# Kernel optimization log

Measured on AMD Instinct MI355X. Metric: run time of the kernel, lower is better.

The kernel has to match this reference:

```python
import jax, jax.numpy as jnp
import numpy as np

BN_EPS = 1e-5


def _fps(xyz, n_centers):
    """Furthest point sampling. xyz: (B,N,3) -> idx (B,n_centers) int32.
    Deterministic start at index 0 (torch version uses randint start)."""
    B, N, _ = xyz.shape
    batch_ar = jnp.arange(B)

    def step(carry, _):
        distances, farthest = carry  # (B,N), (B,)
        center = xyz[batch_ar, farthest]  # (B,3)
        d = jnp.sum((xyz - center[:, None, :]) ** 2, axis=-1)  # (B,N)
        distances = jnp.minimum(distances, d)
        new_far = jnp.argmax(distances, axis=-1)
        return (distances, new_far), farthest

    init = (jnp.full((B, N), jnp.inf, dtype=xyz.dtype),
            jnp.zeros((B,), dtype=jnp.int32))
    _, idxs = jax.lax.scan(step, init, None, length=n_centers)  # (n_centers, B)
    return idxs.T  # (B, n_centers)


def _knn_group(xyz, centers, k):
    """xyz:(B,N,3), centers:(B,M,3) -> patches (B,M,k,3) center-relative."""
    # (B,M,N) squared distances
    dists = jnp.sum((centers[:, :, None, :] - xyz[:, None, :, :]) ** 2, axis=-1)
    _, idx = jax.lax.top_k(-dists, k)  # (B,M,k) smallest distances
    # gather neighbor coords: (B,M,k,3)
    patches = jnp.take_along_axis(xyz[:, None, :, :], idx[..., None], axis=2)
    return patches - centers[:, :, None, :]


def _bn_eval(x, gamma, beta):
    # BatchNorm1d in eval mode: running_mean=0, running_var=1
    return x * (gamma / jnp.sqrt(1.0 + BN_EPS)) + beta


def _mini_pointnet(patches, W1, b1, g1, bt1, W2, b2, g2, bt2, W3, b3, g3, bt3):
    B, M, k, C = patches.shape
    x = patches.reshape(B * M * k, C)
    x = jax.nn.relu(_bn_eval(x @ W1 + b1, g1, bt1))
    x = jax.nn.relu(_bn_eval(x @ W2 + b2, g2, bt2))
    x = jax.nn.relu(_bn_eval(x @ W3 + b3, g3, bt3))
    x = x.reshape(B * M, k, -1).max(axis=1)
    return x.reshape(B, M, -1)


def setup_inputs() -> dict:
    key = jax.random.key(0)
    ks = jax.random.split(key, 8)
    B, N = 16, 16384
    embed = 256

    def lin(kk, fan_in, fan_out):
        bound = 1.0 / np.sqrt(fan_in)
        k1, k2 = jax.random.split(kk)
        W = jax.random.uniform(k1, (fan_in, fan_out), jnp.float32, -bound, bound)
        b = jax.random.uniform(k2, (fan_out,), jnp.float32, -bound, bound)
        return W, b

    W1, b1 = lin(ks[1], 3, 64)
    W2, b2 = lin(ks[2], 64, 128)
    W3, b3 = lin(ks[3], 128, embed)
    return {
        "xyz": jax.random.normal(ks[0], (B, N, 3), jnp.float32),
        "W1": W1, "b1": b1, "g1": jnp.ones((64,)), "bt1": jnp.zeros((64,)),
        "W2": W2, "b2": b2, "g2": jnp.ones((128,)), "bt2": jnp.zeros((128,)),
        "W3": W3, "b3": b3, "g3": jnp.ones((embed,)), "bt3": jnp.zeros((embed,)),
        "n_centers": 256,
        "k": 32,
    }


def reference(xyz, W1, b1, g1, bt1, W2, b2, g2, bt2, W3, b3, g3, bt3,
              n_centers, k):
    center_idx = _fps(xyz, n_centers)  # (B, M)
    centers = jnp.take_along_axis(xyz, center_idx[..., None], axis=1)  # (B,M,3)
    patches = _knn_group(xyz, centers, k)  # (B,M,k,3)
    tokens = _mini_pointnet(patches, W1, b1, g1, bt1, W2, b2, g2, bt2,
                            W3, b3, g3, bt3)
    return tokens, centers
```

## Files before the change

kernel.cpp:

```cpp
#include <hip/hip_runtime.h>

constexpr int B   = 16;
constexpr int N   = 16384;
constexpr int M   = 256;
constexpr int K   = 32;
constexpr int EMB = 256;

__device__ __forceinline__ float sqdist(float px, float py, float pz,
                                        float cx, float cy, float cz) {
  float dx = __fsub_rn(px, cx);
  float dy = __fsub_rn(py, cy);
  float dz = __fsub_rn(pz, cz);
  return __fadd_rn(__fadd_rn(__fmul_rn(dx, dx), __fmul_rn(dy, dy)),
                   __fmul_rn(dz, dz));
}

constexpr int FPS_T = 1024;
constexpr int PPT = N / FPS_T;

__global__ __launch_bounds__(FPS_T) void fps_kernel(
    const float* __restrict__ xyz, float* __restrict__ centers) {
  const int b = blockIdx.x;
  const int tid = threadIdx.x;
  const float* base = xyz + (size_t)b * N * 3;

  float px[PPT], py[PPT], pz[PPT], dist[PPT];
#pragma unroll
  for (int j = 0; j < PPT; ++j) {
    int n = tid + j * FPS_T;
    px[j] = base[n * 3 + 0];
    py[j] = base[n * 3 + 1];
    pz[j] = base[n * 3 + 2];
    dist[j] = __builtin_inff();
  }

  __shared__ float s_c[3];
  __shared__ float s_wv[FPS_T / 64];
  __shared__ int s_wi[FPS_T / 64];
  if (tid == 0) { s_c[0] = base[0]; s_c[1] = base[1]; s_c[2] = base[2]; }
  __syncthreads();

  for (int it = 0; it < M; ++it) {
    const float cx = s_c[0], cy = s_c[1], cz = s_c[2];
    if (tid == 0) {
      float* co = centers + ((size_t)b * M + it) * 3;
      co[0] = cx; co[1] = cy; co[2] = cz;
    }
    float bv = -1.0f;
    int bi = 0x7FFFFFFF;
#pragma unroll
    for (int j = 0; j < PPT; ++j) {
      float d = sqdist(px[j], py[j], pz[j], cx, cy, cz);
      float nd = fminf(dist[j], d);
      dist[j] = nd;
      if (nd > bv) { bv = nd; bi = tid + j * FPS_T; }
    }
#pragma unroll
    for (int mm = 32; mm >= 1; mm >>= 1) {
      float ov = __shfl_xor(bv, mm, 64);
      int oi = __shfl_xor(bi, mm, 64);
      if (ov > bv || (ov == bv && oi < bi)) { bv = ov; bi = oi; }
    }
    if ((tid & 63) == 0) { s_wv[tid >> 6] = bv; s_wi[tid >> 6] = bi; }
    __syncthreads();
    if (tid < 64) {
      float v = (tid < FPS_T / 64) ? s_wv[tid] : -1.0f;
      int i = (tid < FPS_T / 64) ? s_wi[tid] : 0x7FFFFFFF;
#pragma unroll
      for (int mm = 32; mm >= 1; mm >>= 1) {
        float ov = __shfl_xor(v, mm, 64);
        int oi = __shfl_xor(i, mm, 64);
        if (ov > v || (ov == v && oi < i)) { v = ov; i = oi; }
      }
      if (tid == 0) {
        s_c[0] = base[(size_t)i * 3 + 0];
        s_c[1] = base[(size_t)i * 3 + 1];
        s_c[2] = base[(size_t)i * 3 + 2];
      }
    }
    __syncthreads();
  }
}

constexpr int KT = 256;
constexpr int CAP = 512;
constexpr int NBUCKET = 1024;

__global__ __launch_bounds__(KT) void knn_kernel(
    const float* __restrict__ xyz, const float* __restrict__ centers,
    float* __restrict__ patches) {
  const int blk = blockIdx.x;
  const int b = blk >> 8;
  const int tid = threadIdx.x;
  const float* base = xyz + (size_t)b * N * 3;

  __shared__ int hist[NBUCKET];
  __shared__ unsigned cb[CAP];
  __shared__ int ci[CAP];
  __shared__ int s_nin, s_ncand, s_tb;
  __shared__ int s_wsum[KT / 64];
  __shared__ float s_cc[3];

  if (tid == 0) {
    const float* c = centers + (size_t)blk * 3;
    s_cc[0] = c[0]; s_cc[1] = c[1]; s_cc[2] = c[2];
    s_nin = 0; s_ncand = 0;
  }
  for (int i = tid; i < NBUCKET; i += KT) hist[i] = 0;
  __syncthreads();

  const float cx = s_cc[0], cy = s_cc[1], cz = s_cc[2];

  for (int n = tid; n < N; n += KT) {
    float d = sqdist(base[n * 3], base[n * 3 + 1], base[n * 3 + 2], cx, cy, cz);
    atomicAdd(&hist[__float_as_uint(d) >> 21], 1);
  }
  __syncthreads();

  int h0[4];
  int loc = 0;
#pragma unroll
  for (int i = 0; i < 4; ++i) { h0[i] = hist[tid * 4 + i]; loc += h0[i]; }
  int lane = tid & 63, wid = tid >> 6;
  int scan = loc;
  for (int off = 1; off < 64; off <<= 1) {
    int o = __shfl_up(scan, off, 64);
    if (lane >= off) scan += o;
  }
  if (lane == 63) s_wsum[wid] = scan;
  __syncthreads();
  int woff = 0;
  for (int w = 0; w < wid; ++w) woff += s_wsum[w];
  int c0 = woff + scan - loc;
#pragma unroll
  for (int i = 0; i < 4; ++i) {
    int c1 = c0 + h0[i];
    if (c0 < K && c1 >= K) s_tb = tid * 4 + i;
    c0 = c1;
  }
  __syncthreads();
  const int tb = s_tb;
  const unsigned lo = (unsigned)tb << 21;
  const unsigned hi = (unsigned)(tb + 1) << 21;

  for (int n = tid; n < N; n += KT) {
    float x = base[n * 3], y = base[n * 3 + 1], z = base[n * 3 + 2];
    float d = sqdist(x, y, z, cx, cy, cz);
    unsigned bits = __float_as_uint(d);
    if (bits < lo) {
      int pos = atomicAdd(&s_nin, 1);
      float* p = patches + ((size_t)blk * K + pos) * 3;
      p[0] = __fsub_rn(x, cx); p[1] = __fsub_rn(y, cy); p[2] = __fsub_rn(z, cz);
    } else if (bits < hi) {
      int q = atomicAdd(&s_ncand, 1);
      if (q < CAP) { cb[q] = bits; ci[q] = n; }
    }
  }
  __syncthreads();

  const int nin = s_nin;
  const int ncand = min(s_ncand, CAP);
  const int nsel = K - nin;
  for (int j = tid; j < ncand; j += KT) {
    unsigned bj = cb[j];
    int ij = ci[j];
    int rank = 0;
    for (int i2 = 0; i2 < ncand; ++i2) {
      unsigned bv = cb[i2];
      int iv = ci[i2];
      rank += (bv < bj || (bv == bj && iv < ij)) ? 1 : 0;
    }
    if (rank < nsel) {
      float x = base[ij * 3], y = base[ij * 3 + 1], z = base[ij * 3 + 2];
      float* p = patches + ((size_t)blk * K + nin + rank) * 3;
      p[0] = __fsub_rn(x, cx); p[1] = __fsub_rn(y, cy); p[2] = __fsub_rn(z, cz);
    }
  }
}

constexpr int MT = 128;

__global__ __launch_bounds__(MT) void mlp_kernel(
    const float* __restrict__ patches,
    const float* __restrict__ W1, const float* __restrict__ b1,
    const float* __restrict__ g1, const float* __restrict__ bt1,
    const float* __restrict__ W2, const float* __restrict__ b2,
    const float* __restrict__ g2, const float* __restrict__ bt2,
    const float* __restrict__ W3, const float* __restrict__ b3,
    const float* __restrict__ g3, const float* __restrict__ bt3,
    float* __restrict__ tokens) {
  const int pm = blockIdx.x;
  const int tid = threadIdx.x;
  __shared__ float xs[3][K];
  __shared__ float h1s[64 * K];
  __shared__ float h2s[128 * K];
  __shared__ float pms[2][EMB];

  const float* patch = patches + (size_t)pm * (K * 3);
  if (tid < 96) xs[tid % 3][tid / 3] = patch[tid];
  __syncthreads();

  const int cg = tid & 63;
  const int half = tid >> 6;
  const int pt0 = half * 16;
  const float rs = 1.0f / sqrtf(1.0f + 1e-5f);

  {
    const int c = cg;
    const float w0 = W1[c], w1 = W1[64 + c], w2 = W1[128 + c];
    const float bb = b1[c];
    const float sc = g1[c] * rs, be = bt1[c];
    float o[16];
#pragma unroll
    for (int p = 0; p < 16; ++p) {
      int pt = pt0 + p;
      float a = xs[0][pt] * w0 + xs[1][pt] * w1 + xs[2][pt] * w2 + bb;
      o[p] = fmaxf(a * sc + be, 0.0f);
    }
    const int so = (c & 7) << 2;
#pragma unroll
    for (int p4 = 0; p4 < 16; p4 += 4) {
      *(float4*)&h1s[c * K + ((pt0 + p4) ^ so)] =
          make_float4(o[p4], o[p4 + 1], o[p4 + 2], o[p4 + 3]);
    }
  }
  __syncthreads();

  {
    const int c = cg * 2;
    float acc0[16], acc1[16];
    const float bb0 = b2[c], bb1 = b2[c + 1];
#pragma unroll
    for (int p = 0; p < 16; ++p) { acc0[p] = bb0; acc1[p] = bb1; }
    for (int k = 0; k < 64; ++k) {
      const float2 w = *(const float2*)(W2 + k * 128 + c);
      const int so = (k & 7) << 2;
      float4 x0 = *(const float4*)&h1s[k * K + ((pt0 + 0) ^ so)];
      float4 x1 = *(const float4*)&h1s[k * K + ((pt0 + 4) ^ so)];
      float4 x2 = *(const float4*)&h1s[k * K + ((pt0 + 8) ^ so)];
      float4 x3 = *(const float4*)&h1s[k * K + ((pt0 + 12) ^ so)];
      float xv[16] = {x0.x, x0.y, x0.z, x0.w, x1.x, x1.y, x1.z, x1.w,
                      x2.x, x2.y, x2.z, x2.w, x3.x, x3.y, x3.z, x3.w};
#pragma unroll
      for (int p = 0; p < 16; ++p) {
        acc0[p] += xv[p] * w.x;
        acc1[p] += xv[p] * w.y;
      }
    }
    const float sc0 = g2[c] * rs, be0 = bt2[c];
    const float sc1 = g2[c + 1] * rs, be1 = bt2[c + 1];
    float o0[16], o1[16];
#pragma unroll
    for (int p = 0; p < 16; ++p) {
      o0[p] = fmaxf(acc0[p] * sc0 + be0, 0.0f);
      o1[p] = fmaxf(acc1[p] * sc1 + be1, 0.0f);
    }
    const int soa = (c & 7) << 2, sob = ((c + 1) & 7) << 2;
#pragma unroll
    for (int p4 = 0; p4 < 16; p4 += 4) {
      *(float4*)&h2s[c * K + ((pt0 + p4) ^ soa)] =
          make_float4(o0[p4], o0[p4 + 1], o0[p4 + 2], o0[p4 + 3]);
      *(float4*)&h2s[(c + 1) * K + ((pt0 + p4) ^ sob)] =
          make_float4(o1[p4], o1[p4 + 1], o1[p4 + 2], o1[p4 + 3]);
    }
  }
  __syncthreads();

  {
    const int c = cg * 4;
    float acc[4][16];
#pragma unroll
    for (int i = 0; i < 4; ++i) {
      const float bb = b3[c + i];
#pragma unroll
      for (int p = 0; p < 16; ++p) acc[i][p] = bb;
    }
    for (int k = 0; k < 128; ++k) {
      const float4 w = *(const float4*)(W3 + (size_t)k * 256 + c);
      const int so = (k & 7) << 2;
      float4 x0 = *(const float4*)&h2s[k * K + ((pt0 + 0) ^ so)];
      float4 x1 = *(const float4*)&h2s[k * K + ((pt0 + 4) ^ so)];
      float4 x2 = *(const float4*)&h2s[k * K + ((pt0 + 8) ^ so)];
      float4 x3 = *(const float4*)&h2s[k * K + ((pt0 + 12) ^ so)];
      float xv[16] = {x0.x, x0.y, x0.z, x0.w, x1.x, x1.y, x1.z, x1.w,
                      x2.x, x2.y, x2.z, x2.w, x3.x, x3.y, x3.z, x3.w};
#pragma unroll
      for (int p = 0; p < 16; ++p) {
        acc[0][p] += xv[p] * w.x;
        acc[1][p] += xv[p] * w.y;
        acc[2][p] += xv[p] * w.z;
        acc[3][p] += xv[p] * w.w;
      }
    }
#pragma unroll
    for (int i = 0; i < 4; ++i) {
      const float sc = g3[c + i] * rs, be = bt3[c + i];
      float mx = 0.0f;
#pragma unroll
      for (int p = 0; p < 16; ++p)
        mx = fmaxf(mx, fmaxf(acc[i][p] * sc + be, 0.0f));
      pms[half][c + i] = mx;
    }
  }
  __syncthreads();

  {
    const int c2 = tid * 2;
    float* to = tokens + (size_t)pm * EMB;
    to[c2] = fmaxf(pms[0][c2], pms[1][c2]);
    to[c2 + 1] = fmaxf(pms[0][c2 + 1], pms[1][c2 + 1]);
  }
}

extern "C" void kernel_launch(void* const* d_in, const int* in_sizes, int n_in,
                              void* d_out, int out_size, void* d_ws,
                              size_t ws_size, hipStream_t stream) {
  const float* xyz = (const float*)d_in[0];
  const float* W1 = (const float*)d_in[1];
  const float* b1 = (const float*)d_in[2];
  const float* g1 = (const float*)d_in[3];
  const float* bt1 = (const float*)d_in[4];
  const float* W2 = (const float*)d_in[5];
  const float* b2 = (const float*)d_in[6];
  const float* g2 = (const float*)d_in[7];
  const float* bt2 = (const float*)d_in[8];
  const float* W3 = (const float*)d_in[9];
  const float* b3 = (const float*)d_in[10];
  const float* g3 = (const float*)d_in[11];
  const float* bt3 = (const float*)d_in[12];

  float* tokens = (float*)d_out;
  float* centers = tokens + (size_t)B * M * EMB;
  float* patches = (float*)d_ws;

  fps_kernel<<<B, FPS_T, 0, stream>>>(xyz, centers);
  knn_kernel<<<B * M, KT, 0, stream>>>(xyz, centers, patches);
  mlp_kernel<<<B * M, MT, 0, stream>>>(patches, W1, b1, g1, bt1, W2, b2, g2,
                                       bt2, W3, b3, g3, bt3, tokens);
}
```

Before: 863.0 us.

## Cut FPS to one barrier per iteration with double-buffered shared reduction

The furthest-point-sampling kernel now uses 512 threads with 32 points each and double-buffers the per-wave argmax results in shared memory. Every thread redundantly reduces the wave results and loads the new center from global memory, so the second barrier and the shared-memory center broadcast go away. The inner argmax keeps a local slot index chosen by select and computes the global index afterwards. In exchange, more points per thread raise register pressure and every thread does a redundant 8-way reduction and a global load each iteration.

```diff
diff --git a/kernel.cpp b/kernel.cpp
--- a/kernel.cpp
+++ b/kernel.cpp
@@ -15,70 +15,74 @@
                    __fmul_rn(dz, dz));
 }
 
-constexpr int FPS_T = 1024;
-constexpr int PPT = N / FPS_T;
-
-__global__ __launch_bounds__(FPS_T) void fps_kernel(
+constexpr int FT = 512;
+constexpr int FP = N / FT;
+constexpr int FW = FT / 64;
+
+__global__ __launch_bounds__(FT, 2) void fps_kernel(
     const float* __restrict__ xyz, float* __restrict__ centers) {
   const int b = blockIdx.x;
   const int tid = threadIdx.x;
   const float* base = xyz + (size_t)b * N * 3;
 
-  float px[PPT], py[PPT], pz[PPT], dist[PPT];
-#pragma unroll
-  for (int j = 0; j < PPT; ++j) {
-    int n = tid + j * FPS_T;
+  float px[FP], py[FP], pz[FP], dist[FP];
+#pragma unroll
+  for (int j = 0; j < FP; ++j) {
+    int n = tid + j * FT;
     px[j] = base[n * 3 + 0];
     py[j] = base[n * 3 + 1];
     pz[j] = base[n * 3 + 2];
     dist[j] = __builtin_inff();
   }
 
-  __shared__ float s_c[3];
-  __shared__ float s_wv[FPS_T / 64];
-  __shared__ int s_wi[FPS_T / 64];
-  if (tid == 0) { s_c[0] = base[0]; s_c[1] = base[1]; s_c[2] = base[2]; }
-  __syncthreads();
+  __shared__ float s_pv[2][FW];
+  __shared__ int s_pn[2][FW];
+
+  float cx = base[0], cy = base[1], cz = base[2];
 
   for (int it = 0; it < M; ++it) {
-    const float cx = s_c[0], cy = s_c[1], cz = s_c[2];
     if (tid == 0) {
       float* co = centers + ((size_t)b * M + it) * 3;
       co[0] = cx; co[1] = cy; co[2] = cz;
     }
+    const int p = it & 1;
+
     float bv = -1.0f;
-    int bi = 0x7FFFFFFF;
-#pragma unroll
-    for (int j = 0; j < PPT; ++j) {
+    int bj = 0;
+#pragma unroll
+    for (int j = 0; j < FP; ++j) {
       float d = sqdist(px[j], py[j], pz[j], cx, cy, cz);
       float nd = fminf(dist[j], d);
       dist[j] = nd;
-      if (nd > bv) { bv = nd; bi = tid + j * FPS_T; }
-    }
+      bool g = nd > bv;
+      bv = g ? nd : bv;
+      bj = g ? j : bj;
+    }
+    int bn = bj * FT + tid;
+
 #pragma unroll
     for (int mm = 32; mm >= 1; mm >>= 1) {
       float ov = __shfl_xor(bv, mm, 64);
-      int oi = __shfl_xor(bi, mm, 64);
-      if (ov > bv || (ov == bv && oi < bi)) { bv = ov; bi = oi; }
-    }
-    if ((tid & 63) == 0) { s_wv[tid >> 6] = bv; s_wi[tid >> 6] = bi; }
+      int on = __shfl_xor(bn, mm, 64);
+      if (ov > bv || (ov == bv && on < bn)) { bv = ov; bn = on; }
+    }
+    if ((tid & 63) == 0) {
+      s_pv[p][tid >> 6] = bv;
+      s_pn[p][tid >> 6] = bn;
+    }
     __syncthreads();
-    if (tid < 64) {
-      float v = (tid < FPS_T / 64) ? s_wv[tid] : -1.0f;
-      int i = (tid < FPS_T / 64) ? s_wi[tid] : 0x7FFFFFFF;
-#pragma unroll
-      for (int mm = 32; mm >= 1; mm >>= 1) {
-        float ov = __shfl_xor(v, mm, 64);
-        int oi = __shfl_xor(i, mm, 64);
-        if (ov > v || (ov == v && oi < i)) { v = ov; i = oi; }
-      }
-      if (tid == 0) {
-        s_c[0] = base[(size_t)i * 3 + 0];
-        s_c[1] = base[(size_t)i * 3 + 1];
-        s_c[2] = base[(size_t)i * 3 + 2];
-      }
-    }
-    __syncthreads();
+
+    float v = s_pv[p][0];
+    int n = s_pn[p][0];
+#pragma unroll
+    for (int w = 1; w < FW; ++w) {
+      float ov = s_pv[p][w];
+      int on = s_pn[p][w];
+      if (ov > v || (ov == v && on < n)) { v = ov; n = on; }
+    }
+    cx = base[(size_t)n * 3 + 0];
+    cy = base[(size_t)n * 3 + 1];
+    cz = base[(size_t)n * 3 + 2];
   }
 }
 
@@ -333,7 +337,7 @@
   float* centers = tokens + (size_t)B * M * EMB;
   float* patches = (float*)d_ws;
 
-  fps_kernel<<<B, FPS_T, 0, stream>>>(xyz, centers);
+  fps_kernel<<<B, FT, 0, stream>>>(xyz, centers);
   knn_kernel<<<B * M, KT, 0, stream>>>(xyz, centers, patches);
   mlp_kernel<<<B * M, MT, 0, stream>>>(patches, W1, b1, g1, bt1, W2, b2, g2,
                                        bt2, W3, b3, g3, bt3, tokens);
```

Result: faster. 813.4 us (-5.8%).
